# Kernel tuning notes

Hardware: AMD Instinct MI355X
Metric: run time of the kernel (lower is better)

Reference implementation:

```python
import jax, jax.numpy as jnp
import numpy as np
import math

D = 768
H = 8
DH = D // H
T = 4
MODES = 16
NUM_CLASSES = 14


def setup_inputs() -> dict:
    key = jax.random.key(0)
    ks = iter(jax.random.split(key, 64))
    B, S = 256, 512
    inp = {}
    inp['x_feat'] = jax.random.normal(next(ks), (B, S, D), dtype=jnp.float32)
    # attention pool
    inp['pool_w'] = jax.random.normal(next(ks), (D, 1), dtype=jnp.float32) * 0.02
    inp['pool_b'] = jnp.zeros((1,), dtype=jnp.float32)
    # per-block params, stacked over T
    def pstack(shape, scale=0.02):
        return jax.random.normal(next(ks), (T,) + shape, dtype=jnp.float32) * scale
    inp['w_q'] = pstack((D, D)); inp['w_k'] = pstack((D, D)); inp['w_v'] = pstack((D, D))
    inp['b_qkv'] = jnp.zeros((T, 3 * D), dtype=jnp.float32)
    inp['w_o'] = pstack((D, D)); inp['b_o'] = jnp.zeros((T, D), dtype=jnp.float32)
    inp['ln1_g'] = jnp.ones((T, D), dtype=jnp.float32); inp['ln1_b'] = jnp.zeros((T, D), dtype=jnp.float32)
    inp['ln2_g'] = jnp.ones((T, D), dtype=jnp.float32); inp['ln2_b'] = jnp.zeros((T, D), dtype=jnp.float32)
    inp['scale_real'] = pstack((MODES, D)); inp['scale_imag'] = pstack((MODES, D))
    inp['proj_w'] = pstack((D, D)); inp['proj_b'] = jnp.zeros((T, D), dtype=jnp.float32)
    inp['bn_g'] = jnp.ones((T, D), dtype=jnp.float32); inp['bn_b'] = jnp.zeros((T, D), dtype=jnp.float32)
    inp['gate'] = jnp.full((T,), 0.5, dtype=jnp.float32)
    inp['scale_attn'] = jnp.ones((T,), dtype=jnp.float32)
    inp['scale_denoise'] = jnp.ones((T,), dtype=jnp.float32)
    # fuse MLP + classifier
    inp['f1_w'] = jax.random.normal(next(ks), (D, 256), dtype=jnp.float32) * 0.02
    inp['f1_b'] = jnp.zeros((256,), dtype=jnp.float32)
    inp['f1_bn_g'] = jnp.ones((256,), dtype=jnp.float32); inp['f1_bn_b'] = jnp.zeros((256,), dtype=jnp.float32)
    inp['f2_w'] = jax.random.normal(next(ks), (256, 128), dtype=jnp.float32) * 0.02
    inp['f2_b'] = jnp.zeros((128,), dtype=jnp.float32)
    inp['f2_bn_g'] = jnp.ones((128,), dtype=jnp.float32); inp['f2_bn_b'] = jnp.zeros((128,), dtype=jnp.float32)
    inp['cls_w'] = jax.random.normal(next(ks), (128, NUM_CLASSES), dtype=jnp.float32) * 0.02
    inp['cls_b'] = jnp.zeros((NUM_CLASSES,), dtype=jnp.float32)
    return inp


def _layernorm(x, g, b, eps=1e-5):
    mu = jnp.mean(x, axis=-1, keepdims=True)
    var = jnp.var(x, axis=-1, keepdims=True)
    return (x - mu) * jax.lax.rsqrt(var + eps) * g + b


def _bn_eval(x, g, b, eps=1e-5):
    # eval-mode BatchNorm1d with running_mean=0, running_var=1
    return x * (g / jnp.sqrt(1.0 + eps)) + b


def _forward(x_feat, pool_w, pool_b, w_q, w_k, w_v, b_qkv, w_o, b_o,
             ln1_g, ln1_b, ln2_g, ln2_b, scale_real, scale_imag, proj_w, proj_b,
             bn_g, bn_b, gate, scale_attn, scale_denoise,
             f1_w, f1_b, f1_bn_g, f1_bn_b, f2_w, f2_b, f2_bn_g, f2_bn_b,
             cls_w, cls_b):
    B, S, _ = x_feat.shape
    # attention pool: softmax over seq of a scalar score per token
    scores = x_feat @ pool_w + pool_b          # [B,S,1]
    weights = jax.nn.softmax(scores, axis=1)
    z = jnp.sum(weights * x_feat, axis=1)      # [B,D]

    def classify(z):
        h = jax.nn.relu(_bn_eval(z @ f1_w + f1_b, f1_bn_g, f1_bn_b))
        h = jax.nn.relu(_bn_eval(h @ f2_w + f2_b, f2_bn_g, f2_bn_b))
        return h @ cls_w + cls_b

    logits_sum = jnp.zeros((B, NUM_CLASSES), dtype=x_feat.dtype)
    for t in range(T):
        bq, bk, bv = b_qkv[t, :D], b_qkv[t, D:2 * D], b_qkv[t, 2 * D:]
        # query: single token z [B,1,D]; keys/values: x_feat [B,S,D]
        q = (z @ w_q[t].T + bq).reshape(B, H, 1, DH)
        k = (x_feat @ w_k[t].T + bk).reshape(B, S, H, DH).transpose(0, 2, 1, 3)
        v = (x_feat @ w_v[t].T + bv).reshape(B, S, H, DH).transpose(0, 2, 1, 3)
        att = jax.nn.softmax(jnp.einsum('bhqd,bhsd->bhqs', q, k) / math.sqrt(DH), axis=-1)
        o = jnp.einsum('bhqs,bhsd->bhqd', att, v).reshape(B, D)
        z_attn = o @ w_o[t].T + b_o[t]
        z1 = _layernorm(z + scale_attn[t] * z_attn, ln1_g[t], ln1_b[t])
        # fft denoise: keep first MODES freq bins scaled by mean of complex filter per mode
        z_freq = jnp.fft.fft(z1, axis=1)                        # [B,D] complex
        filt = jnp.mean(scale_real[t] + 1j * scale_imag[t], axis=1)  # [MODES] complex
        keep = z_freq[:, :MODES] * filt[None, :]
        z_filtered = jnp.concatenate([keep, jnp.zeros((B, D - MODES), dtype=z_freq.dtype)], axis=1)
        z_spatial = jnp.fft.ifft(z_filtered, axis=1).real
        z_den = z_spatial @ proj_w[t].T + proj_b[t]
        z2 = _layernorm(z1 + scale_denoise[t] * z_den, ln2_g[t], ln2_b[t])
        g = jax.nn.sigmoid(gate[t])
        z3 = g * z2 + (1.0 - g) * z
        z = _bn_eval(z3, bn_g[t], bn_b[t])
        logits_sum = logits_sum + classify(z)
    return logits_sum / T


def reference(x_feat, pool_w, pool_b, w_q, w_k, w_v, b_qkv, w_o, b_o,
              ln1_g, ln1_b, ln2_g, ln2_b, scale_real, scale_imag, proj_w, proj_b,
              bn_g, bn_b, gate, scale_attn, scale_denoise,
              f1_w, f1_b, f1_bn_g, f1_bn_b, f2_w, f2_b, f2_bn_g, f2_bn_b,
              cls_w, cls_b):
    return _forward(x_feat, pool_w, pool_b, w_q, w_k, w_v, b_qkv, w_o, b_o,
                    ln1_g, ln1_b, ln2_g, ln2_b, scale_real, scale_imag, proj_w, proj_b,
                    bn_g, bn_b, gate, scale_attn, scale_denoise,
                    f1_w, f1_b, f1_bn_g, f1_bn_b, f2_w, f2_b, f2_bn_g, f2_bn_b,
                    cls_w, cls_b)
```

## Files before the change

kernel.cpp:

```cpp
#include <hip/hip_runtime.h>
#include <math.h>


#define DEV __device__ __forceinline__

typedef unsigned int   uint32;
typedef unsigned short ushort_t;
typedef __attribute__((ext_vector_type(8))) short bf16x8;
typedef __attribute__((ext_vector_type(4))) float f32x4;
typedef __attribute__((ext_vector_type(2))) float f32x2;

constexpr int Bv  = 256;
constexpr int Sv  = 512;
constexpr int Dv  = 768;
constexpr int Hv  = 8;
constexpr int DHv = 96;
constexpr int NCv = 14;

constexpr size_t ZL  = 196608;
constexpr size_t XWL = 1572864;
constexpr size_t WL  = 2359296;
constexpr size_t WT  = 589824;

DEV float4 ld4(const float* p) { return *reinterpret_cast<const float4*>(p); }

DEV ushort_t f2bf(float f) {
    uint32 u = __float_as_uint(f);
    u += 0x7FFFu + ((u >> 16) & 1u);
    return (ushort_t)(u >> 16);
}
DEV float bf2f(ushort_t h) { return __uint_as_float((uint32)h << 16); }
DEV void split2(float f, ushort_t& hi, ushort_t& lo) {
    hi = f2bf(f);
    lo = f2bf(f - bf2f(hi));
}
DEV uint2 pack4(float4 v) {
    return make_uint2((uint32)f2bf(v.x) | ((uint32)f2bf(v.y) << 16),
                      (uint32)f2bf(v.z) | ((uint32)f2bf(v.w) << 16));
}

DEV f32x2 bfpair(uint32 u) {
    f32x2 r;
    r.x = __uint_as_float(u << 16);
    r.y = __uint_as_float(u & 0xFFFF0000u);
    return r;
}

DEV f32x2 pkfma(f32x2 a, f32x2 b, f32x2 c) {
    f32x2 d;
    asm("v_pk_fma_f32 %0, %1, %2, %3" : "=v"(d) : "v"(a), "v"(b), "v"(c));
    return d;
}

DEV void glds16(const void* g, void* l) {
    __builtin_amdgcn_global_load_lds(
        (const __attribute__((address_space(1))) void*)g,
        (__attribute__((address_space(3))) void*)l, 16, 0, 0);
}

__global__ __launch_bounds__(512, 4)
void pool_cvt_kernel(const float* __restrict__ x, const float* __restrict__ pool_w,
                     ushort_t* __restrict__ xbf,
                     float* __restrict__ pacc, float2* __restrict__ pml)
{
    __shared__ float qks[Dv];
    const int b = blockIdx.x, half = blockIdx.y;
    const int tid = threadIdx.x, wave = tid >> 6, lane = tid & 63;
    for (int i = tid; i < Dv / 4; i += 512)
        *reinterpret_cast<float4*>(&qks[i * 4]) = ld4(pool_w + i * 4);
    __syncthreads();

    const int row0 = half * 256 + wave * 32;
    const float* base = x + ((size_t)b * Sv + row0) * Dv + 4 * lane;

    float4 acc[3];
#pragma unroll
    for (int j = 0; j < 3; ++j) acc[j] = make_float4(0.f, 0.f, 0.f, 0.f);
    float m = -INFINITY, l = 0.f;

    float4 c0[3], c1[3];
#pragma unroll
    for (int j = 0; j < 3; ++j) { c0[j] = ld4(base + 256 * j); c1[j] = ld4(base + Dv + 256 * j); }

    for (int it = 0; it < 16; ++it) {
        float4 n0_[3], n1_[3];
        if (it < 15) {
            const float* nb = base + (size_t)(2 * it + 2) * Dv;
#pragma unroll
            for (int j = 0; j < 3; ++j) { n0_[j] = ld4(nb + 256 * j); n1_[j] = ld4(nb + Dv + 256 * j); }
        }
        ushort_t* ob = xbf + ((size_t)b * Sv + row0 + 2 * it) * Dv + 4 * lane;
#pragma unroll
        for (int j = 0; j < 3; ++j) *reinterpret_cast<uint2*>(ob + 256 * j) = pack4(c0[j]);
#pragma unroll
        for (int j = 0; j < 3; ++j) *reinterpret_cast<uint2*>(ob + Dv + 256 * j) = pack4(c1[j]);
        float p0 = 0.f, p1 = 0.f;
#pragma unroll
        for (int j = 0; j < 3; ++j) {
            const float4 q4 = *reinterpret_cast<const float4*>(&qks[4 * lane + 256 * j]);
            p0 = fmaf(q4.x, c0[j].x, p0); p0 = fmaf(q4.y, c0[j].y, p0);
            p0 = fmaf(q4.z, c0[j].z, p0); p0 = fmaf(q4.w, c0[j].w, p0);
            p1 = fmaf(q4.x, c1[j].x, p1); p1 = fmaf(q4.y, c1[j].y, p1);
            p1 = fmaf(q4.z, c1[j].z, p1); p1 = fmaf(q4.w, c1[j].w, p1);
        }
#pragma unroll
        for (int dd = 1; dd < 64; dd <<= 1) { p0 += __shfl_xor(p0, dd); p1 += __shfl_xor(p1, dd); }
        float mx = fmaxf(p0, p1);
        if (mx > m) {
            float r = __expf(m - mx); l *= r;
#pragma unroll
            for (int j = 0; j < 3; ++j) { acc[j].x *= r; acc[j].y *= r; acc[j].z *= r; acc[j].w *= r; }
            m = mx;
        }
        float w0 = __expf(p0 - m), w1 = __expf(p1 - m);
        l += w0 + w1;
#pragma unroll
        for (int j = 0; j < 3; ++j) {
            acc[j].x = fmaf(w1, c1[j].x, fmaf(w0, c0[j].x, acc[j].x));
            acc[j].y = fmaf(w1, c1[j].y, fmaf(w0, c0[j].y, acc[j].y));
            acc[j].z = fmaf(w1, c1[j].z, fmaf(w0, c0[j].z, acc[j].z));
            acc[j].w = fmaf(w1, c1[j].w, fmaf(w0, c0[j].w, acc[j].w));
        }
        if (it < 15) {
#pragma unroll
            for (int j = 0; j < 3; ++j) { c0[j] = n0_[j]; c1[j] = n1_[j]; }
        }
    }
    const int p = half * 8 + wave;
    const size_t pidx = (size_t)p * 256 + b;
#pragma unroll
    for (int j = 0; j < 3; ++j)
        *reinterpret_cast<float4*>(&pacc[pidx * Dv + 4 * lane + 256 * j]) = acc[j];
    if (lane == 0) pml[pidx] = make_float2(m, l);
}

__global__ __launch_bounds__(512, 4)
void attn_flash_kernel(const ushort_t* __restrict__ xbf, const float* __restrict__ Qk,
                       float* __restrict__ pacc, float2* __restrict__ pml, float scale)
{
    const int b = blockIdx.x, half = blockIdx.y;
    const int tid = threadIdx.x, wave = tid >> 6, lane = tid & 63;
    const int hg = wave & 3, slice = wave >> 2;
    const int h0 = 2 * hg, h1 = h0 + 1;
    const int row0 = half * 256 + slice * 128;

    f32x2 q0[6], q1[6];
    {
        const float* qp0 = Qk + ((size_t)b * Hv + h0) * Dv + 4 * lane;
        const float* qp1 = Qk + ((size_t)b * Hv + h1) * Dv + 4 * lane;
#pragma unroll
        for (int s = 0; s < 3; ++s) {
            float4 a = ld4(qp0 + s * 256);
            float4 c = ld4(qp1 + s * 256);
            q0[2 * s]     = (f32x2){a.x, a.y}; q0[2 * s + 1] = (f32x2){a.z, a.w};
            q1[2 * s]     = (f32x2){c.x, c.y}; q1[2 * s + 1] = (f32x2){c.z, c.w};
        }
    }
    f32x2 a0[6], a1[6];
#pragma unroll
    for (int c = 0; c < 6; ++c) { a0[c] = (f32x2){0.f, 0.f}; a1[c] = (f32x2){0.f, 0.f}; }
    float m0 = -INFINITY, l0 = 0.f, m1 = -INFINITY, l1 = 0.f;

    const ushort_t* base = xbf + ((size_t)b * Sv + row0) * Dv + 4 * lane;

    uint2 c0[3], c1[3];
#pragma unroll
    for (int s = 0; s < 3; ++s) {
        c0[s] = *reinterpret_cast<const uint2*>(base + s * 256);
        c1[s] = *reinterpret_cast<const uint2*>(base + Dv + s * 256);
    }

    for (int it = 0; it < 64; ++it) {
        __builtin_amdgcn_s_barrier();
        uint2 n0[3], n1[3];
        if (it < 63) {
            const ushort_t* nb = base + (size_t)(2 * it + 2) * Dv;
#pragma unroll
            for (int s = 0; s < 3; ++s) {
                n0[s] = *reinterpret_cast<const uint2*>(nb + s * 256);
                n1[s] = *reinterpret_cast<const uint2*>(nb + Dv + s * 256);
            }
        }
        f32x2 xf0[6], xf1[6];
#pragma unroll
        for (int s = 0; s < 3; ++s) {
            xf0[2 * s] = bfpair(c0[s].x); xf0[2 * s + 1] = bfpair(c0[s].y);
            xf1[2 * s] = bfpair(c1[s].x); xf1[2 * s + 1] = bfpair(c1[s].y);
        }
        f32x2 t00 = (f32x2){0.f, 0.f}, t01 = t00, t10 = t00, t11 = t00;
#pragma unroll
        for (int c = 0; c < 6; ++c) {
            t00 = pkfma(xf0[c], q0[c], t00);
            t01 = pkfma(xf0[c], q1[c], t01);
            t10 = pkfma(xf1[c], q0[c], t10);
            t11 = pkfma(xf1[c], q1[c], t11);
        }
        float s4[4];
        s4[0] = t00.x + t00.y;
        s4[1] = t01.x + t01.y;
        s4[2] = t10.x + t10.y;
        s4[3] = t11.x + t11.y;
        {
            const bool k0 = (lane & 1), k1 = (lane & 2);
            float sd0 = k0 ? s4[0] : s4[1];
            float rc0 = __shfl_xor(sd0, 1);
            float t0  = (k0 ? s4[1] : s4[0]) + rc0;
            float sd1 = k0 ? s4[2] : s4[3];
            float rc1 = __shfl_xor(sd1, 1);
            float t1  = (k0 ? s4[3] : s4[2]) + rc1;
            float sd2 = k1 ? t0 : t1;
            float rc2 = __shfl_xor(sd2, 2);
            float u   = (k1 ? t1 : t0) + rc2;
            u += __shfl_xor(u, 4);  u += __shfl_xor(u, 8);
            u += __shfl_xor(u, 16); u += __shfl_xor(u, 32);
            float b1 = __shfl_xor(u, 1);
            float b2 = __shfl_xor(u, 2);
            float b3 = __shfl_xor(u, 3);
            s4[0] = k1 ? (k0 ? b3 : b2) : (k0 ? b1 : u);
            s4[1] = k1 ? (k0 ? b2 : b3) : (k0 ? u  : b1);
            s4[2] = k1 ? (k0 ? b1 : u ) : (k0 ? b3 : b2);
            s4[3] = k1 ? (k0 ? u  : b1) : (k0 ? b2 : b3);
        }
#pragma unroll
        for (int j = 0; j < 4; ++j) s4[j] *= scale;
        {
            float mx = fmaxf(s4[0], s4[2]);
            if (mx > m0) {
                float f = __expf(m0 - mx); l0 *= f;
#pragma unroll
                for (int c = 0; c < 6; ++c) { a0[c].x *= f; a0[c].y *= f; }
                m0 = mx;
            }
            float w0 = __expf(s4[0] - m0), w1 = __expf(s4[2] - m0);
            l0 += w0 + w1;
            f32x2 w02 = (f32x2){w0, w0}, w12 = (f32x2){w1, w1};
#pragma unroll
            for (int c = 0; c < 6; ++c) a0[c] = pkfma(xf1[c], w12, pkfma(xf0[c], w02, a0[c]));
        }
        {
            float mx = fmaxf(s4[1], s4[3]);
            if (mx > m1) {
                float f = __expf(m1 - mx); l1 *= f;
#pragma unroll
                for (int c = 0; c < 6; ++c) { a1[c].x *= f; a1[c].y *= f; }
                m1 = mx;
            }
            float w0 = __expf(s4[1] - m1), w1 = __expf(s4[3] - m1);
            l1 += w0 + w1;
            f32x2 w02 = (f32x2){w0, w0}, w12 = (f32x2){w1, w1};
#pragma unroll
            for (int c = 0; c < 6; ++c) a1[c] = pkfma(xf1[c], w12, pkfma(xf0[c], w02, a1[c]));
        }
        if (it < 63) {
#pragma unroll
            for (int s = 0; s < 3; ++s) { c0[s] = n0[s]; c1[s] = n1[s]; }
        }
    }

    const int p = half * 2 + slice;
    const size_t pidx0 = ((size_t)p * 256 + b) * Hv + h0;
    const size_t pidx1 = pidx0 + 1;
    float* pb0 = pacc + pidx0 * Dv + 4 * lane;
    float* pb1 = pacc + pidx1 * Dv + 4 * lane;
#pragma unroll
    for (int s = 0; s < 3; ++s) {
        *reinterpret_cast<float4*>(pb0 + s * 256) =
            make_float4(a0[2 * s].x, a0[2 * s].y, a0[2 * s + 1].x, a0[2 * s + 1].y);
        *reinterpret_cast<float4*>(pb1 + s * 256) =
            make_float4(a1[2 * s].x, a1[2 * s].y, a1[2 * s + 1].x, a1[2 * s + 1].y);
    }
    if (lane == 0) {
        pml[pidx0] = make_float2(m0, l0);
        pml[pidx1] = make_float2(m1, l1);
    }
}

template<int NH, int NP, bool WF32>
__global__ __launch_bounds__(256)
void merge_kernel(const float* __restrict__ pacc, const float2* __restrict__ pml,
                  ushort_t* __restrict__ obf, size_t loOff, float* __restrict__ of32)
{
    __shared__ float eS[NH * NP];
    const int b = blockIdx.x, tid = threadIdx.x;
    if (tid < NH) {
        float2 mls[NP];
        float mm = -INFINITY;
#pragma unroll
        for (int p = 0; p < NP; ++p) {
            mls[p] = pml[((size_t)p * 256 + b) * NH + tid];
            mm = fmaxf(mm, mls[p].x);
        }
        float ee[NP]; float L = 0.f;
#pragma unroll
        for (int p = 0; p < NP; ++p) { ee[p] = __expf(mls[p].x - mm); L += mls[p].y * ee[p]; }
        float inv = 1.f / L;
#pragma unroll
        for (int p = 0; p < NP; ++p) eS[tid * NP + p] = ee[p] * inv;
    }
    __syncthreads();
#pragma unroll
    for (int seg = 0; seg < NH * 3; ++seg) {
        int h = seg / 3;
        int d = (seg - h * 3) * 256 + tid;
        float v = 0.f;
#pragma unroll
        for (int p = 0; p < NP; ++p)
            v += pacc[((size_t)((size_t)p * 256 + b) * NH + h) * Dv + d] * eS[h * NP + p];
        size_t oi = ((size_t)b * NH + h) * Dv + d;
        ushort_t hi, lo; split2(v, hi, lo);
        obf[oi] = hi; obf[oi + loOff] = lo;
        if (WF32) of32[oi] = v;
    }
}

template<int MODE, bool OBF>
__global__ __launch_bounds__(256)
void mgemm_kernel(const ushort_t* __restrict__ A, size_t aLo,
                  const ushort_t* __restrict__ W, size_t wLo,
                  const float* __restrict__ bias, void* __restrict__ outp,
                  size_t oLo)
{
    constexpr int BN = (MODE == 2) ? 96 : 64;
    constexpr int BK = (MODE == 1) ? 32 : 64;
    constexpr int NJ = BN / 32;
    constexpr int KTOT = (MODE == 1) ? 96 : 768;
    constexpr int NSTEP = KTOT / BK;
    constexpr int CH = BK / 8;
    constexpr int CA = (64 * BK) / 512;
    constexpr int CB = (BN * BK) / 512;
    constexpr int NC = 2 * (CA + CB) / 4;
    constexpr int LDA = (MODE == 2) ? 6144 : 768;
    constexpr int LDW = (MODE == 1) ? 96 : 768;
    constexpr int LDO = (MODE == 1) ? 6144 : 768;
    constexpr int WCW = (MODE == 2) ? 48 : 32;
    constexpr int RSH = (BK == 64) ? 7 : 6;

    __shared__ ushort_t As[2][2][64 * BK];
    __shared__ ushort_t Bs[2][2][BN * BK];

    const int tid = threadIdx.x, wave = tid >> 6, lane = tid & 63;
    const int n0 = blockIdx.x * BN;
    const int m0 = blockIdx.y * 64;
    const int h  = (MODE == 1) ? blockIdx.z : ((MODE == 2) ? blockIdx.x : 0);
    const int acol = (MODE == 1) ? h * 96 : ((MODE == 2) ? h * 768 : 0);
    const ushort_t* Wb = W + ((MODE == 1) ? (size_t)h * 768 * 96 : (size_t)0);
    const int ocol = (MODE == 1) ? h * 768 : 0;

    const int wr = wave >> 1, wc = wave & 1;
    const int l15 = lane & 15, kg = lane >> 4;

    auto stage = [&](int kt, int buf) {
#pragma unroll
        for (int hl = 0; hl < 2; ++hl) {
            const ushort_t* Ap = A + (hl ? aLo : 0);
            const ushort_t* Wp = Wb + (hl ? wLo : 0);
#pragma unroll
            for (int c = 0; c < CA / 4; ++c) {
                int call = wave + 4 * c;
                int off = call * 1024 + lane * 16;
                int row = off >> RSH;
                int chunk = (off & (2 * BK - 1)) >> 4;
                int sw = chunk ^ (row & (CH - 1));
                const ushort_t* src = Ap + (size_t)(m0 + row) * LDA + acol + kt + sw * 8;
                glds16(src, (char*)As[buf][hl] + call * 1024);
            }
#pragma unroll
            for (int c = 0; c < CB / 4; ++c) {
                int call = wave + 4 * c;
                int off = call * 1024 + lane * 16;
                int row = off >> RSH;
                int chunk = (off & (2 * BK - 1)) >> 4;
                int sw = chunk ^ (row & (CH - 1));
                const ushort_t* src = Wp + (size_t)(n0 + row) * LDW + kt + sw * 8;
                glds16(src, (char*)Bs[buf][hl] + call * 1024);
            }
        }
    };

    f32x4 acc[2][NJ];
#pragma unroll
    for (int i = 0; i < 2; ++i)
#pragma unroll
        for (int j = 0; j < NJ; ++j) acc[i][j] = (f32x4){0.f, 0.f, 0.f, 0.f};

    stage(0, 0);
    int cur = 0;
    for (int s = 0; s < NSTEP; ++s) {
        __builtin_amdgcn_s_barrier();
        if (s + 1 < NSTEP) {
            stage((s + 1) * BK, cur ^ 1);
            asm volatile("s_waitcnt vmcnt(%0)" :: "i"(NC) : "memory");
        } else {
            asm volatile("s_waitcnt vmcnt(0)" ::: "memory");
        }
        __builtin_amdgcn_s_barrier();
        __builtin_amdgcn_sched_barrier(0);

        const ushort_t* ah_ = As[cur][0];
        const ushort_t* al_ = As[cur][1];
        const ushort_t* bh_ = Bs[cur][0];
        const ushort_t* bl_ = Bs[cur][1];
#pragma unroll
        for (int kw = 0; kw < BK / 32; ++kw) {
            const int kb = kw * 4;
            bf16x8 ah[2], al[2], bh[NJ], bl[NJ];
#pragma unroll
            for (int i = 0; i < 2; ++i) {
                int r = wr * 32 + i * 16 + l15;
                int c = (kb + kg) ^ (r & (CH - 1));
                ah[i] = *reinterpret_cast<const bf16x8*>(&ah_[r * BK + c * 8]);
                al[i] = *reinterpret_cast<const bf16x8*>(&al_[r * BK + c * 8]);
            }
#pragma unroll
            for (int j = 0; j < NJ; ++j) {
                int r = wc * WCW + j * 16 + l15;
                int c = (kb + kg) ^ (r & (CH - 1));
                bh[j] = *reinterpret_cast<const bf16x8*>(&bh_[r * BK + c * 8]);
                bl[j] = *reinterpret_cast<const bf16x8*>(&bl_[r * BK + c * 8]);
            }
#pragma unroll
            for (int i = 0; i < 2; ++i)
#pragma unroll
                for (int j = 0; j < NJ; ++j) {
                    acc[i][j] = __builtin_amdgcn_mfma_f32_16x16x32_bf16(al[i], bh[j], acc[i][j], 0, 0, 0);
                    acc[i][j] = __builtin_amdgcn_mfma_f32_16x16x32_bf16(ah[i], bl[j], acc[i][j], 0, 0, 0);
                    acc[i][j] = __builtin_amdgcn_mfma_f32_16x16x32_bf16(ah[i], bh[j], acc[i][j], 0, 0, 0);
                }
        }
        cur ^= 1;
    }

#pragma unroll
    for (int i = 0; i < 2; ++i)
#pragma unroll
        for (int j = 0; j < NJ; ++j) {
            int rg = m0 + wr * 32 + i * 16 + kg * 4;
            int cg = n0 + wc * WCW + j * 16 + l15;
            float bv = bias ? bias[cg] : 0.f;
#pragma unroll
            for (int reg = 0; reg < 4; ++reg) {
                float v = acc[i][j][reg] + bv;
                size_t oi = (size_t)(rg + reg) * LDO + ocol + cg;
                if (OBF) {
                    ushort_t hi, lo; split2(v, hi, lo);
                    ((ushort_t*)outp)[oi] = hi;
                    ((ushort_t*)outp)[oi + oLo] = lo;
                } else {
                    ((float*)outp)[oi] = v;
                }
            }
        }
}

__global__ __launch_bounds__(256)
void cvt3_kernel(const float* __restrict__ wq, const float* __restrict__ wv,
                 const float* __restrict__ wo, ushort_t* __restrict__ dst)
{
    const int bid = blockIdx.x;
    const int w = bid / 1152;
    const int off = (bid - w * 1152) * 2048 + threadIdx.x * 8;
    const float* src = (w == 0) ? wq : (w == 1) ? wv : wo;
    ushort_t hi[8], lo[8];
#pragma unroll
    for (int e = 0; e < 8; ++e) split2(src[off + e], hi[e], lo[e]);
    ushort_t* base = dst + (size_t)w * (2 * WL);
    *reinterpret_cast<uint4*>(base + off) = *reinterpret_cast<uint4*>(hi);
    *reinterpret_cast<uint4*>(base + WL + off) = *reinterpret_cast<uint4*>(lo);
}

__global__ __launch_bounds__(256)
void wkT_kernel(const float* __restrict__ w_k, ushort_t* __restrict__ wkT)
{
    __shared__ float tile[96][65];
    const int n0 = blockIdx.x * 64;
    const int th = blockIdx.y;
    const int t = th >> 3, h = th & 7;
    const float* src = w_k + ((size_t)t * Dv + h * DHv) * Dv + n0;
    for (int idx = threadIdx.x; idx < 96 * 64; idx += 256) {
        int j = idx >> 6, n = idx & 63;
        tile[j][n] = src[(size_t)j * Dv + n];
    }
    __syncthreads();
    for (int idx = threadIdx.x; idx < 64 * 96; idx += 256) {
        int n = idx / 96, j = idx - n * 96;
        ushort_t hi, lo; split2(tile[j][n], hi, lo);
        size_t oi = ((size_t)th * Dv + n0 + n) * DHv + j;
        wkT[oi] = hi; wkT[oi + WL] = lo;
    }
}

__global__ __launch_bounds__(256)
void pre1_kernel(float* __restrict__ twc, float* __restrict__ tws,
                 const float* __restrict__ sr, const float* __restrict__ si,
                 float* __restrict__ filt)
{
    __shared__ float red[8];
    const int bid = blockIdx.x;
    if (bid < 48) {
        int idx = bid * 256 + threadIdx.x;
        int k = idx / Dv, n = idx % Dv;
        int r = (k * n) % Dv;
        float ang = (float)r * (float)(6.283185307179586 / 768.0);
        twc[idx] = cosf(ang);
        tws[idx] = sinf(ang);
    } else {
        int tk = bid - 48;
        const float* a  = sr + (size_t)tk * Dv;
        const float* b2 = si + (size_t)tk * Dv;
        float s1 = 0.f, s2 = 0.f;
#pragma unroll
        for (int j = 0; j < 3; ++j) {
            int c = threadIdx.x + 256 * j;
            s1 += a[c]; s2 += b2[c];
        }
        int wave = threadIdx.x >> 6, lane = threadIdx.x & 63;
#pragma unroll
        for (int dd = 1; dd < 64; dd <<= 1) { s1 += __shfl_xor(s1, dd); s2 += __shfl_xor(s2, dd); }
        if (lane == 0) { red[wave * 2] = s1; red[wave * 2 + 1] = s2; }
        __syncthreads();
        if (threadIdx.x == 0) {
            filt[tk * 2]     = (red[0] + red[2] + red[4] + red[6]) * (1.f / 768.f);
            filt[tk * 2 + 1] = (red[1] + red[3] + red[5] + red[7]) * (1.f / 768.f);
        }
    }
}

__global__ __launch_bounds__(256)
void cs_kernel(const float* __restrict__ proj_w, const float* __restrict__ twc,
               const float* __restrict__ tws, float* __restrict__ csC,
               float* __restrict__ csS)
{
    const int wave = threadIdx.x >> 6, lane = threadIdx.x & 63;
    const int gw = blockIdx.x * 4 + wave;
    const int t = gw / 768;
    const int i = gw - t * 768;
    const float* pr = proj_w + ((size_t)t * Dv + i) * Dv + 4 * lane;
    float4 p4[3];
#pragma unroll
    for (int j = 0; j < 3; ++j) p4[j] = ld4(pr + 256 * j);
    for (int k = 0; k < 16; ++k) {
        const float* tc = twc + (size_t)k * Dv + 4 * lane;
        const float* ts = tws + (size_t)k * Dv + 4 * lane;
        float ac = 0.f, as = 0.f;
#pragma unroll
        for (int j = 0; j < 3; ++j) {
            float4 c4 = ld4(tc + 256 * j);
            float4 s4 = ld4(ts + 256 * j);
            ac = fmaf(p4[j].x, c4.x, ac); ac = fmaf(p4[j].y, c4.y, ac);
            ac = fmaf(p4[j].z, c4.z, ac); ac = fmaf(p4[j].w, c4.w, ac);
            as = fmaf(p4[j].x, s4.x, as); as = fmaf(p4[j].y, s4.y, as);
            as = fmaf(p4[j].z, s4.z, as); as = fmaf(p4[j].w, s4.w, as);
        }
#pragma unroll
        for (int dd = 1; dd < 64; dd <<= 1) {
            ac += __shfl_xor(ac, dd);
            as += __shfl_xor(as, dd);
        }
        if (lane == 0) {
            csC[((size_t)t * 16 + k) * Dv + i] = ac * (1.f / 768.f);
            csS[((size_t)t * 16 + k) * Dv + i] = as * (1.f / 768.f);
        }
    }
}

__global__ __launch_bounds__(256)
void lnden_kernel(float* __restrict__ z, ushort_t* __restrict__ zbf,
                  const float* __restrict__ za,
                  const float* __restrict__ g1, const float* __restrict__ b1,
                  const float* __restrict__ g2, const float* __restrict__ b2,
                  const float* __restrict__ bng, const float* __restrict__ bnb,
                  const float* __restrict__ gate_p, const float* __restrict__ sa_p,
                  const float* __restrict__ sd_p,
                  const float* __restrict__ twc, const float* __restrict__ tws,
                  const float* __restrict__ filt_t,
                  const float* __restrict__ csC_t, const float* __restrict__ csS_t,
                  const float* __restrict__ pb_t,
                  const float* __restrict__ f1w, const float* __restrict__ f1b,
                  const float* __restrict__ f1g, const float* __restrict__ f1bb,
                  const float* __restrict__ f2w, const float* __restrict__ f2b,
                  const float* __restrict__ f2g, const float* __restrict__ f2bb,
                  const float* __restrict__ clw, const float* __restrict__ clb,
                  float* __restrict__ outp, int t)
{
    const int b = blockIdx.x, tid = threadIdx.x;
    const int wave = tid >> 6, lane = tid & 63;
    __shared__ float red[8];
    __shared__ float dred[4][32];
    __shared__ float fin[32];
    __shared__ float kr[16], ki[16];
    __shared__ float zs[768];
    __shared__ float h1s[256];
    __shared__ float h2s[128];

    const float sa = sa_p[0];
    float v[3], zo[3];
    float s = 0.f, s2 = 0.f;
#pragma unroll
    for (int j = 0; j < 3; ++j) {
        int c = tid + 256 * j;
        zo[j] = z[(size_t)b * Dv + c];
        float val = zo[j] + sa * za[(size_t)b * Dv + c];
        v[j] = val; s += val; s2 += val * val;
    }
#pragma unroll
    for (int dd = 1; dd < 64; dd <<= 1) { s += __shfl_xor(s, dd); s2 += __shfl_xor(s2, dd); }
    if (lane == 0) { red[wave * 2] = s; red[wave * 2 + 1] = s2; }
    __syncthreads();
    {
        const float mean = (red[0] + red[2] + red[4] + red[6]) * (1.f / 768.f);
        const float var  = (red[1] + red[3] + red[5] + red[7]) * (1.f / 768.f) - mean * mean;
        const float rstd = rsqrtf(var + 1e-5f);
#pragma unroll
        for (int j = 0; j < 3; ++j) {
            int c = tid + 256 * j;
            v[j] = (v[j] - mean) * rstd * g1[c] + b1[c];
        }
    }
    float Fc[16], Fs[16];
#pragma unroll
    for (int k = 0; k < 16; ++k) { Fc[k] = 0.f; Fs[k] = 0.f; }
#pragma unroll
    for (int j = 0; j < 3; ++j) {
        int c = tid + 256 * j;
#pragma unroll
        for (int k = 0; k < 16; ++k) {
            Fc[k] = fmaf(v[j], twc[k * Dv + c], Fc[k]);
            Fs[k] = fmaf(v[j], tws[k * Dv + c], Fs[k]);
        }
    }
#pragma unroll
    for (int dd = 1; dd < 64; dd <<= 1) {
#pragma unroll
        for (int k = 0; k < 16; ++k) { Fc[k] += __shfl_xor(Fc[k], dd); Fs[k] += __shfl_xor(Fs[k], dd); }
    }
    if (lane == 0) {
#pragma unroll
        for (int k = 0; k < 16; ++k) { dred[wave][k] = Fc[k]; dred[wave][16 + k] = Fs[k]; }
    }
    __syncthreads();
    if (tid < 32) fin[tid] = dred[0][tid] + dred[1][tid] + dred[2][tid] + dred[3][tid];
    __syncthreads();
    if (tid < 16) {
        float Sc = fin[tid], Ss = fin[16 + tid];
        float fr = filt_t[tid * 2], fi = filt_t[tid * 2 + 1];
        kr[tid] = Sc * fr + Ss * fi;
        ki[tid] = Sc * fi - Ss * fr;
    }
    __syncthreads();

    const float sd  = sd_p[0];
    const float gv  = 1.f / (1.f + expf(-gate_p[0]));
    const float bnc = 1.f / sqrtf(1.f + 1e-5f);
    float w3[3];
    s = 0.f; s2 = 0.f;
#pragma unroll
    for (int j = 0; j < 3; ++j) {
        int c = tid + 256 * j;
        float den = pb_t[c];
#pragma unroll
        for (int k = 0; k < 16; ++k) {
            den = fmaf(kr[k], csC_t[k * Dv + c], den);
            den = fmaf(-ki[k], csS_t[k * Dv + c], den);
        }
        float val = v[j] + sd * den;
        w3[j] = val; s += val; s2 += val * val;
    }
#pragma unroll
    for (int dd = 1; dd < 64; dd <<= 1) { s += __shfl_xor(s, dd); s2 += __shfl_xor(s2, dd); }
    if (lane == 0) { red[wave * 2] = s; red[wave * 2 + 1] = s2; }
    __syncthreads();
    const float mean2 = (red[0] + red[2] + red[4] + red[6]) * (1.f / 768.f);
    const float var2  = (red[1] + red[3] + red[5] + red[7]) * (1.f / 768.f) - mean2 * mean2;
    const float rstd2 = rsqrtf(var2 + 1e-5f);
#pragma unroll
    for (int j = 0; j < 3; ++j) {
        int c = tid + 256 * j;
        float z2v = (w3[j] - mean2) * rstd2 * g2[c] + b2[c];
        float z3v = gv * z2v + (1.f - gv) * zo[j];
        float zn  = z3v * (bng[c] * bnc) + bnb[c];
        z[(size_t)b * Dv + c] = zn;
        ushort_t hi, lo; split2(zn, hi, lo);
        zbf[(size_t)b * Dv + c] = hi;
        zbf[(size_t)b * Dv + c + ZL] = lo;
        zs[c] = zn;
    }
    __syncthreads();
    {
        float h0 = f1b[tid], h1 = 0.f, h2 = 0.f, h3 = 0.f;
        for (int d = 0; d < 768; d += 4) {
            h0 = fmaf(zs[d],     f1w[(size_t)d * 256 + tid], h0);
            h1 = fmaf(zs[d + 1], f1w[(size_t)(d + 1) * 256 + tid], h1);
            h2 = fmaf(zs[d + 2], f1w[(size_t)(d + 2) * 256 + tid], h2);
            h3 = fmaf(zs[d + 3], f1w[(size_t)(d + 3) * 256 + tid], h3);
        }
        float h = (h0 + h1) + (h2 + h3);
        h = h * (f1g[tid] * bnc) + f1bb[tid];
        h1s[tid] = fmaxf(h, 0.f);
    }
    __syncthreads();
    if (tid < 128) {
        float h0 = f2b[tid], h1 = 0.f, h2 = 0.f, h3 = 0.f;
        for (int i2 = 0; i2 < 256; i2 += 4) {
            h0 = fmaf(h1s[i2],     f2w[(size_t)i2 * 128 + tid], h0);
            h1 = fmaf(h1s[i2 + 1], f2w[(size_t)(i2 + 1) * 128 + tid], h1);
            h2 = fmaf(h1s[i2 + 2], f2w[(size_t)(i2 + 2) * 128 + tid], h2);
            h3 = fmaf(h1s[i2 + 3], f2w[(size_t)(i2 + 3) * 128 + tid], h3);
        }
        float h2v = ((h0 + h1) + (h2 + h3)) * (f2g[tid] * bnc) + f2bb[tid];
        h2s[tid] = fmaxf(h2v, 0.f);
    }
    __syncthreads();
    if (tid < NCv) {
        float lg = clb[tid];
        for (int i2 = 0; i2 < 128; ++i2) lg = fmaf(h2s[i2], clw[(size_t)i2 * NCv + tid], lg);
        lg *= 0.25f;
        if (t == 0) outp[(size_t)b * NCv + tid] = lg;
        else        outp[(size_t)b * NCv + tid] += lg;
    }
}

extern "C" void kernel_launch(void* const* d_in, const int* in_sizes, int n_in,
                              void* d_out, int out_size, void* d_ws, size_t ws_size,
                              hipStream_t stream)
{
    (void)in_sizes; (void)n_in; (void)out_size; (void)ws_size;
    const float* x      = (const float*)d_in[0];
    const float* pool_w = (const float*)d_in[1];
    const float* w_q   = (const float*)d_in[3];
    const float* w_k   = (const float*)d_in[4];
    const float* w_v   = (const float*)d_in[5];
    const float* b_qkv = (const float*)d_in[6];
    const float* w_o   = (const float*)d_in[7];
    const float* b_o   = (const float*)d_in[8];
    const float* ln1_g = (const float*)d_in[9];
    const float* ln1_b = (const float*)d_in[10];
    const float* ln2_g = (const float*)d_in[11];
    const float* ln2_b = (const float*)d_in[12];
    const float* s_re  = (const float*)d_in[13];
    const float* s_im  = (const float*)d_in[14];
    const float* proj_w= (const float*)d_in[15];
    const float* proj_b= (const float*)d_in[16];
    const float* bn_g  = (const float*)d_in[17];
    const float* bn_b  = (const float*)d_in[18];
    const float* gate  = (const float*)d_in[19];
    const float* s_at  = (const float*)d_in[20];
    const float* s_dn  = (const float*)d_in[21];
    const float* f1w   = (const float*)d_in[22];
    const float* f1b   = (const float*)d_in[23];
    const float* f1g   = (const float*)d_in[24];
    const float* f1bb  = (const float*)d_in[25];
    const float* f2w   = (const float*)d_in[26];
    const float* f2b   = (const float*)d_in[27];
    const float* f2g   = (const float*)d_in[28];
    const float* f2bb  = (const float*)d_in[29];
    const float* clw   = (const float*)d_in[30];
    const float* clb   = (const float*)d_in[31];
    float* out = (float*)d_out;

    float* ws   = (float*)d_ws;
    float* twc  = ws;
    float* tws  = twc + 12288;
    float* filt = tws + 12288;
    float* csC  = filt + 128;
    float* csS  = csC + 49152;
    float* z    = csS + 49152;
    float* za   = z + 196608;
    float* Qk   = za + 196608;
    float* pacc = Qk + 1572864;
    float* pmlf = pacc + 6291456;
    ushort_t* xbf  = (ushort_t*)(pmlf + 16384);
    ushort_t* zbf  = xbf + 100663296;
    ushort_t* qbf  = zbf + 2 * ZL;
    ushort_t* xwbf = qbf + 2 * ZL;
    ushort_t* obf  = xwbf + 2 * XWL;
    ushort_t* wspl = obf + 2 * ZL;
    ushort_t* wkT  = wspl + 6 * WL;
    float2* pml = (float2*)pmlf;
    ushort_t* wqbf = wspl;
    ushort_t* wvbf = wspl + 2 * WL;
    ushort_t* wobf = wspl + 4 * WL;

    pre1_kernel<<<112, 256, 0, stream>>>(twc, tws, s_re, s_im, filt);
    cs_kernel<<<768, 256, 0, stream>>>(proj_w, twc, tws, csC, csS);
    cvt3_kernel<<<3456, 256, 0, stream>>>(w_q, w_v, w_o, wspl);
    wkT_kernel<<<dim3(12, 32), 256, 0, stream>>>(w_k, wkT);

    pool_cvt_kernel<<<dim3(256, 2), 512, 0, stream>>>(x, pool_w, xbf, pacc, pml);
    merge_kernel<1, 16, true><<<256, 256, 0, stream>>>(pacc, pml, zbf, ZL, z);

    const float iscale = (float)(1.0 / sqrt(96.0));
    for (int t = 0; t < 4; ++t) {
        mgemm_kernel<0, true><<<dim3(12, 4), 256, 0, stream>>>(
            zbf, ZL, wqbf + (size_t)t * WT, WL, b_qkv + (size_t)t * 2304, qbf, ZL);
        mgemm_kernel<1, false><<<dim3(12, 4, 8), 256, 0, stream>>>(
            qbf, ZL, wkT + (size_t)t * WT, WL, nullptr, Qk, 0);
        attn_flash_kernel<<<dim3(256, 2), 512, 0, stream>>>(xbf, Qk, pacc, pml, iscale);
        merge_kernel<8, 4, false><<<256, 256, 0, stream>>>(pacc, pml, xwbf, XWL, nullptr);
        mgemm_kernel<2, true><<<dim3(8, 4), 256, 0, stream>>>(
            xwbf, XWL, wvbf + (size_t)t * WT, WL, b_qkv + (size_t)t * 2304 + 1536, obf, ZL);
        mgemm_kernel<0, false><<<dim3(12, 4), 256, 0, stream>>>(
            obf, ZL, wobf + (size_t)t * WT, WL, b_o + (size_t)t * Dv, za, 0);
        lnden_kernel<<<256, 256, 0, stream>>>(
            z, zbf, za,
            ln1_g + (size_t)t * Dv, ln1_b + (size_t)t * Dv,
            ln2_g + (size_t)t * Dv, ln2_b + (size_t)t * Dv,
            bn_g + (size_t)t * Dv, bn_b + (size_t)t * Dv,
            gate + t, s_at + t, s_dn + t,
            twc, tws, filt + (size_t)t * 32,
            csC + (size_t)t * 12288, csS + (size_t)t * 12288,
            proj_b + (size_t)t * Dv,
            f1w, f1b, f1g, f1bb, f2w, f2b, f2g, f2bb,
            clw, clb, out, t);
    }
}
```

Baseline: 950.8 us.

## Assign one head per wave in attention pooling and halve partial splits

```diff
diff --git a/kernel.cpp b/kernel.cpp
--- a/kernel.cpp
+++ b/kernel.cpp
@@ -134,145 +134,81 @@
     if (lane == 0) pml[pidx] = make_float2(m, l);
 }
 
-__global__ __launch_bounds__(512, 4)
+__global__ __launch_bounds__(512, 7)
 void attn_flash_kernel(const ushort_t* __restrict__ xbf, const float* __restrict__ Qk,
                        float* __restrict__ pacc, float2* __restrict__ pml, float scale)
 {
     const int b = blockIdx.x, half = blockIdx.y;
     const int tid = threadIdx.x, wave = tid >> 6, lane = tid & 63;
-    const int hg = wave & 3, slice = wave >> 2;
-    const int h0 = 2 * hg, h1 = h0 + 1;
-    const int row0 = half * 256 + slice * 128;
-
-    f32x2 q0[6], q1[6];
+    const int h = wave;
+    const int row0 = half * 256;
+
+    f32x2 q[6];
     {
-        const float* qp0 = Qk + ((size_t)b * Hv + h0) * Dv + 4 * lane;
-        const float* qp1 = Qk + ((size_t)b * Hv + h1) * Dv + 4 * lane;
+        const float* qp = Qk + ((size_t)b * Hv + h) * Dv + 4 * lane;
 #pragma unroll
         for (int s = 0; s < 3; ++s) {
-            float4 a = ld4(qp0 + s * 256);
-            float4 c = ld4(qp1 + s * 256);
-            q0[2 * s]     = (f32x2){a.x, a.y}; q0[2 * s + 1] = (f32x2){a.z, a.w};
-            q1[2 * s]     = (f32x2){c.x, c.y}; q1[2 * s + 1] = (f32x2){c.z, c.w};
-        }
-    }
-    f32x2 a0[6], a1[6];
-#pragma unroll
-    for (int c = 0; c < 6; ++c) { a0[c] = (f32x2){0.f, 0.f}; a1[c] = (f32x2){0.f, 0.f}; }
-    float m0 = -INFINITY, l0 = 0.f, m1 = -INFINITY, l1 = 0.f;
+            float4 a = ld4(qp + s * 256);
+            q[2 * s]     = (f32x2){a.x, a.y};
+            q[2 * s + 1] = (f32x2){a.z, a.w};
+        }
+    }
+    f32x2 acc[6];
+#pragma unroll
+    for (int c = 0; c < 6; ++c) acc[c] = (f32x2){0.f, 0.f};
+    float m = -INFINITY, l = 0.f;
 
     const ushort_t* base = xbf + ((size_t)b * Sv + row0) * Dv + 4 * lane;
 
-    uint2 c0[3], c1[3];
-#pragma unroll
-    for (int s = 0; s < 3; ++s) {
-        c0[s] = *reinterpret_cast<const uint2*>(base + s * 256);
-        c1[s] = *reinterpret_cast<const uint2*>(base + Dv + s * 256);
-    }
-
-    for (int it = 0; it < 64; ++it) {
-        __builtin_amdgcn_s_barrier();
-        uint2 n0[3], n1[3];
-        if (it < 63) {
-            const ushort_t* nb = base + (size_t)(2 * it + 2) * Dv;
-#pragma unroll
-            for (int s = 0; s < 3; ++s) {
-                n0[s] = *reinterpret_cast<const uint2*>(nb + s * 256);
-                n1[s] = *reinterpret_cast<const uint2*>(nb + Dv + s * 256);
-            }
-        }
-        f32x2 xf0[6], xf1[6];
+    uint2 c0[3];
+#pragma unroll
+    for (int s = 0; s < 3; ++s) c0[s] = *reinterpret_cast<const uint2*>(base + s * 256);
+
+    for (int it = 0; it < 256; ++it) {
+        uint2 n0[3];
+        if (it < 255) {
+            const ushort_t* nb = base + (size_t)(it + 1) * Dv;
+#pragma unroll
+            for (int s = 0; s < 3; ++s) n0[s] = *reinterpret_cast<const uint2*>(nb + s * 256);
+        }
+        f32x2 xf[6];
 #pragma unroll
         for (int s = 0; s < 3; ++s) {
-            xf0[2 * s] = bfpair(c0[s].x); xf0[2 * s + 1] = bfpair(c0[s].y);
-            xf1[2 * s] = bfpair(c1[s].x); xf1[2 * s + 1] = bfpair(c1[s].y);
-        }
-        f32x2 t00 = (f32x2){0.f, 0.f}, t01 = t00, t10 = t00, t11 = t00;
-#pragma unroll
-        for (int c = 0; c < 6; ++c) {
-            t00 = pkfma(xf0[c], q0[c], t00);
-            t01 = pkfma(xf0[c], q1[c], t01);
-            t10 = pkfma(xf1[c], q0[c], t10);
-            t11 = pkfma(xf1[c], q1[c], t11);
-        }
-        float s4[4];
-        s4[0] = t00.x + t00.y;
-        s4[1] = t01.x + t01.y;
-        s4[2] = t10.x + t10.y;
-        s4[3] = t11.x + t11.y;
-        {
-            const bool k0 = (lane & 1), k1 = (lane & 2);
-            float sd0 = k0 ? s4[0] : s4[1];
-            float rc0 = __shfl_xor(sd0, 1);
-            float t0  = (k0 ? s4[1] : s4[0]) + rc0;
-            float sd1 = k0 ? s4[2] : s4[3];
-            float rc1 = __shfl_xor(sd1, 1);
-            float t1  = (k0 ? s4[3] : s4[2]) + rc1;
-            float sd2 = k1 ? t0 : t1;
-            float rc2 = __shfl_xor(sd2, 2);
-            float u   = (k1 ? t1 : t0) + rc2;
-            u += __shfl_xor(u, 4);  u += __shfl_xor(u, 8);
-            u += __shfl_xor(u, 16); u += __shfl_xor(u, 32);
-            float b1 = __shfl_xor(u, 1);
-            float b2 = __shfl_xor(u, 2);
-            float b3 = __shfl_xor(u, 3);
-            s4[0] = k1 ? (k0 ? b3 : b2) : (k0 ? b1 : u);
-            s4[1] = k1 ? (k0 ? b2 : b3) : (k0 ? u  : b1);
-            s4[2] = k1 ? (k0 ? b1 : u ) : (k0 ? b3 : b2);
-            s4[3] = k1 ? (k0 ? u  : b1) : (k0 ? b2 : b3);
-        }
-#pragma unroll
-        for (int j = 0; j < 4; ++j) s4[j] *= scale;
-        {
-            float mx = fmaxf(s4[0], s4[2]);
-            if (mx > m0) {
-                float f = __expf(m0 - mx); l0 *= f;
-#pragma unroll
-                for (int c = 0; c < 6; ++c) { a0[c].x *= f; a0[c].y *= f; }
-                m0 = mx;
-            }
-            float w0 = __expf(s4[0] - m0), w1 = __expf(s4[2] - m0);
-            l0 += w0 + w1;
-            f32x2 w02 = (f32x2){w0, w0}, w12 = (f32x2){w1, w1};
-#pragma unroll
-            for (int c = 0; c < 6; ++c) a0[c] = pkfma(xf1[c], w12, pkfma(xf0[c], w02, a0[c]));
-        }
-        {
-            float mx = fmaxf(s4[1], s4[3]);
-            if (mx > m1) {
-                float f = __expf(m1 - mx); l1 *= f;
-#pragma unroll
-                for (int c = 0; c < 6; ++c) { a1[c].x *= f; a1[c].y *= f; }
-                m1 = mx;
-            }
-            float w0 = __expf(s4[1] - m1), w1 = __expf(s4[3] - m1);
-            l1 += w0 + w1;
-            f32x2 w02 = (f32x2){w0, w0}, w12 = (f32x2){w1, w1};
-#pragma unroll
-            for (int c = 0; c < 6; ++c) a1[c] = pkfma(xf1[c], w12, pkfma(xf0[c], w02, a1[c]));
-        }
-        if (it < 63) {
-#pragma unroll
-            for (int s = 0; s < 3; ++s) { c0[s] = n0[s]; c1[s] = n1[s]; }
-        }
-    }
-
-    const int p = half * 2 + slice;
-    const size_t pidx0 = ((size_t)p * 256 + b) * Hv + h0;
-    const size_t pidx1 = pidx0 + 1;
-    float* pb0 = pacc + pidx0 * Dv + 4 * lane;
-    float* pb1 = pacc + pidx1 * Dv + 4 * lane;
-#pragma unroll
-    for (int s = 0; s < 3; ++s) {
-        *reinterpret_cast<float4*>(pb0 + s * 256) =
-            make_float4(a0[2 * s].x, a0[2 * s].y, a0[2 * s + 1].x, a0[2 * s + 1].y);
-        *reinterpret_cast<float4*>(pb1 + s * 256) =
-            make_float4(a1[2 * s].x, a1[2 * s].y, a1[2 * s + 1].x, a1[2 * s + 1].y);
-    }
-    if (lane == 0) {
-        pml[pidx0] = make_float2(m0, l0);
-        pml[pidx1] = make_float2(m1, l1);
-    }
+            xf[2 * s]     = bfpair(c0[s].x);
+            xf[2 * s + 1] = bfpair(c0[s].y);
+        }
+        f32x2 t = (f32x2){0.f, 0.f};
+#pragma unroll
+        for (int c = 0; c < 6; ++c) t = pkfma(xf[c], q[c], t);
+        float s1 = t.x + t.y;
+#pragma unroll
+        for (int dd = 1; dd < 64; dd <<= 1) s1 += __shfl_xor(s1, dd);
+        s1 *= scale;
+        if (s1 > m) {
+            float f = __expf(m - s1);
+            l *= f;
+#pragma unroll
+            for (int c = 0; c < 6; ++c) { acc[c].x *= f; acc[c].y *= f; }
+            m = s1;
+        }
+        float w = __expf(s1 - m);
+        l += w;
+        f32x2 w2 = (f32x2){w, w};
+#pragma unroll
+        for (int c = 0; c < 6; ++c) acc[c] = pkfma(xf[c], w2, acc[c]);
+        if (it < 255) {
+#pragma unroll
+            for (int s = 0; s < 3; ++s) c0[s] = n0[s];
+        }
+    }
+
+    const size_t pidx = ((size_t)half * 256 + b) * Hv + h;
+    float* pb = pacc + pidx * Dv + 4 * lane;
+#pragma unroll
+    for (int s = 0; s < 3; ++s)
+        *reinterpret_cast<float4*>(pb + s * 256) =
+            make_float4(acc[2 * s].x, acc[2 * s].y, acc[2 * s + 1].x, acc[2 * s + 1].y);
+    if (lane == 0) pml[pidx] = make_float2(m, l);
 }
 
 template<int NH, int NP, bool WF32>
@@ -795,7 +731,7 @@
         mgemm_kernel<1, false><<<dim3(12, 4, 8), 256, 0, stream>>>(
             qbf, ZL, wkT + (size_t)t * WT, WL, nullptr, Qk, 0);
         attn_flash_kernel<<<dim3(256, 2), 512, 0, stream>>>(xbf, Qk, pacc, pml, iscale);
-        merge_kernel<8, 4, false><<<256, 256, 0, stream>>>(pacc, pml, xwbf, XWL, nullptr);
+        merge_kernel<8, 2, false><<<256, 256, 0, stream>>>(pacc, pml, xwbf, XWL, nullptr);
         mgemm_kernel<2, true><<<dim3(8, 4), 256, 0, stream>>>(
             xwbf, XWL, wvbf + (size_t)t * WT, WL, b_qkv + (size_t)t * 2304 + 1536, obf, ZL);
         mgemm_kernel<0, false><<<dim3(12, 4), 256, 0, stream>>>(
```

After: 1.143 ms. 20.2% more time.
